# Performance work log

Measured on AMD Instinct MI355X. Metric: run time of the kernel, lower is better.

Reference implementation:

```python
import jax, jax.numpy as jnp
import numpy as np
from jax import lax

SCOPE = 15
RICKER_WIDTH = 3.0
DAMP = 0.12
MAX_STEPS = 10


def mexican_hat(scope, width, damping):
    # ricker / mexican-hat wavelet sampled at `scope` integer-spaced points, scaled by damping
    x = np.linspace(-(scope // 2), scope // 2, scope).astype(np.float32)
    norm = 2.0 / (np.sqrt(3.0 * width) * np.pi ** 0.25)
    w = damping * norm * (1.0 - (x / width) ** 2) * np.exp(-(x ** 2) / (2.0 * width ** 2))
    return jnp.asarray(w, dtype=jnp.float32)


def setup_inputs() -> dict:
    key = jax.random.key(0)
    activations = jax.random.normal(key, (32, 256, 56, 56), dtype=jnp.float32)
    w_rec = mexican_hat(SCOPE, RICKER_WIDTH, DAMP)  # [scope]
    return {"activations": activations, "w_rec": w_rec, "max_steps": MAX_STEPS}


def reference(activations, w_rec, max_steps):
    # activations: [B, C, H, W]; inhibition conv runs along the C axis only.
    scope = w_rec.shape[0]
    pad = scope // 2
    x = activations[:, None]                     # [B, 1, C, H, W]
    kernel = w_rec.reshape(1, 1, scope, 1, 1)    # OIDHW

    def conv(y):
        return lax.conv_general_dilated(
            y, kernel,
            window_strides=(1, 1, 1),
            padding=[(pad, pad), (0, 0), (0, 0)],
            dimension_numbers=("NCDHW", "OIDHW", "NCDHW"),
        )

    # fixed-point iteration: state <- activations + W_rec * state  (threshold=0 => always max_steps iters)
    state = x
    for _ in range(max_steps):
        state = x + conv(state)
    return state[:, 0]  # squeeze channel dim -> [B, C, H, W]
```

## Files before the change

kernel.cpp:

```cpp
#include <hip/hip_runtime.h>


#define NCH 256
#define PAD 7
#define SCOPE 15
#define SPATIAL 3136
#define PER_B 802816
#define STW 32
#define STILES_PER_B 98
#define NTILES 3136
#define GRID_APPLY 512
#define MAXCH 12

typedef __attribute__((ext_vector_type(8))) __bf16 bf16x8;
typedef __attribute__((ext_vector_type(16))) float float16;
typedef __attribute__((ext_vector_type(4))) unsigned int uint4v;

static __device__ __forceinline__ unsigned short f2bf_rn_u(float f) {
  unsigned u = __builtin_bit_cast(unsigned int, f);
  return (unsigned short)((u + 0x7FFFu + ((u >> 16) & 1u)) >> 16);
}
static __device__ __forceinline__ float bf2f_u(unsigned short h) {
  unsigned u = ((unsigned)h) << 16;
  return __builtin_bit_cast(float, u);
}
static __device__ __forceinline__ unsigned pack_bf2(float a, float b) {
  return (unsigned)f2bf_rn_u(a) | ((unsigned)f2bf_rn_u(b) << 16);
}
static __device__ __forceinline__ void split2(float a, float b,
                                              unsigned& h, unsigned& l) {
  h = pack_bf2(a, b);
  const float ra = a - __builtin_bit_cast(float, h << 16);
  const float rb = b - __builtin_bit_cast(float, h & 0xFFFF0000u);
  l = pack_bf2(ra, rb);
}

__global__ void build_M_kernel(const float* __restrict__ w,
                               const int* __restrict__ max_steps_p,
                               unsigned short* __restrict__ Mh,
                               unsigned short* __restrict__ Ml) {
  const int d = blockIdx.x;
  const int c = threadIdx.x;
  __shared__ float v[2][NCH];
  __shared__ float wsh[SCOPE];
  if (c < SCOPE) wsh[c] = w[c];
  const float e = (c == d) ? 1.0f : 0.0f;
  v[0][c] = e;
  __syncthreads();
  const int steps = *max_steps_p;
  int cur = 0;
  for (int t = 0; t < steps; ++t) {
    float s = e;
#pragma unroll
    for (int j = 0; j < SCOPE; ++j) {
      const int cc = c + j - PAD;
      if (cc >= 0 && cc < NCH) s += wsh[j] * v[cur][cc];
    }
    cur ^= 1;
    v[cur][c] = s;
    __syncthreads();
  }
  const float f = v[cur][c];
  const unsigned short h = f2bf_rn_u(f);
  Mh[c * NCH + d] = h;
  Ml[c * NCH + d] = f2bf_rn_u(f - bf2f_u(h));
}

__global__ __launch_bounds__(512, 4) void apply_M_kernel(
    const float* __restrict__ x, const unsigned short* __restrict__ Mh,
    const unsigned short* __restrict__ Ml, float* __restrict__ out) {
  __shared__ unsigned HB[128 * STW];
  __shared__ unsigned LB[128 * STW];

  const int tid  = threadIdx.x;
  const int lane = tid & 63;
  const int w    = tid >> 6;
  const int m    = lane & 31;
  const int half = lane >> 5;
  const int c0   = w * 32;

  int clo = c0 - 70; if (clo < 0) clo = 0; clo >>= 4;
  int chi = c0 + 101; if (chi > 255) chi = 255; chi >>= 4;
  const int nch = chi - clo + 1;

  const unsigned short* mh = Mh + (c0 + m) * NCH + clo * 16 + half * 8;
  const unsigned short* ml = Ml + (c0 + m) * NCH + clo * 16 + half * 8;

  const int sq = (tid & 7) * 4;
  const int dg = tid >> 3;

  int tau = blockIdx.x;
  float4 g0, g1, g2, g3;
  {
    const float* gb = x + (size_t)(tau / STILES_PER_B) * PER_B
                        + (size_t)(tau % STILES_PER_B) * STW;
    g0 = *(const float4*)(gb + (size_t)(2 * dg) * SPATIAL + sq);
    g1 = *(const float4*)(gb + (size_t)(2 * dg + 1) * SPATIAL + sq);
    g2 = *(const float4*)(gb + (size_t)(2 * dg + 128) * SPATIAL + sq);
    g3 = *(const float4*)(gb + (size_t)(2 * dg + 129) * SPATIAL + sq);
  }

#pragma unroll 1
  for (; tau < NTILES; tau += GRID_APPLY) {
    __syncthreads();

    {
      unsigned h0, h1, h2, h3, l0, l1, l2, l3;
      split2(g0.x, g1.x, h0, l0); split2(g0.y, g1.y, h1, l1);
      split2(g0.z, g1.z, h2, l2); split2(g0.w, g1.w, h3, l3);
      *(uint4v*)&HB[dg * STW + sq] = (uint4v){h0, h1, h2, h3};
      *(uint4v*)&LB[dg * STW + sq] = (uint4v){l0, l1, l2, l3};
      split2(g2.x, g3.x, h0, l0); split2(g2.y, g3.y, h1, l1);
      split2(g2.z, g3.z, h2, l2); split2(g2.w, g3.w, h3, l3);
      *(uint4v*)&HB[(dg + 64) * STW + sq] = (uint4v){h0, h1, h2, h3};
      *(uint4v*)&LB[(dg + 64) * STW + sq] = (uint4v){l0, l1, l2, l3};
    }

    const int ntau = tau + GRID_APPLY;
    if (ntau < NTILES) {
      const float* gb = x + (size_t)(ntau / STILES_PER_B) * PER_B
                          + (size_t)(ntau % STILES_PER_B) * STW;
      g0 = *(const float4*)(gb + (size_t)(2 * dg) * SPATIAL + sq);
      g1 = *(const float4*)(gb + (size_t)(2 * dg + 1) * SPATIAL + sq);
      g2 = *(const float4*)(gb + (size_t)(2 * dg + 128) * SPATIAL + sq);
      g3 = *(const float4*)(gb + (size_t)(2 * dg + 129) * SPATIAL + sq);
    }

    __syncthreads();

    const unsigned short* mhp = mh;
    const unsigned short* mlp = ml;
    asm volatile("" : "+v"(mhp), "+v"(mlp));

    float16 a0, a1;
#pragma unroll
    for (int q = 0; q < 16; ++q) { a0[q] = 0.0f; a1[q] = 0.0f; }

#pragma unroll
    for (int i = 0; i < MAXCH; ++i) {
      if (i < nch) {
        const bf16x8 Ah = *(const bf16x8*)(mhp + i * 16);
        const bf16x8 Al = *(const bf16x8*)(mlp + i * 16);
        const int k2b = (clo + i) * 8 + half * 4;
        const unsigned* hp = &HB[k2b * STW + m];
        const unsigned* lp = &LB[k2b * STW + m];
        const uint4v hw = {hp[0], hp[32], hp[64], hp[96]};
        const uint4v lw = {lp[0], lp[32], lp[64], lp[96]};
        const bf16x8 bh = __builtin_bit_cast(bf16x8, hw);
        const bf16x8 bl = __builtin_bit_cast(bf16x8, lw);
        a0 = __builtin_amdgcn_mfma_f32_32x32x16_bf16(Ah, bh, a0, 0, 0, 0);
        a1 = __builtin_amdgcn_mfma_f32_32x32x16_bf16(Ah, bl, a1, 0, 0, 0);
        a1 = __builtin_amdgcn_mfma_f32_32x32x16_bf16(Al, bh, a1, 0, 0, 0);
      }
    }

    const int b  = tau / STILES_PER_B;
    const int s0 = (tau % STILES_PER_B) * STW;
    float* ob = out + (size_t)b * PER_B + (size_t)s0 + m;
#pragma unroll
    for (int r = 0; r < 16; ++r) {
      const int row = (r & 3) + 8 * (r >> 2) + 4 * half;
      ob[(size_t)(c0 + row) * SPATIAL] = a0[r] + a1[r];
    }
  }
}

extern "C" void kernel_launch(void* const* d_in, const int* in_sizes, int n_in,
                              void* d_out, int out_size, void* d_ws, size_t ws_size,
                              hipStream_t stream) {
  const float* x = (const float*)d_in[0];
  const float* w = (const float*)d_in[1];
  const int* ms = (const int*)d_in[2];
  float* out = (float*)d_out;

  unsigned short* Mh = (unsigned short*)d_ws;
  unsigned short* Ml = Mh + NCH * NCH;

  build_M_kernel<<<NCH, NCH, 0, stream>>>(w, ms, Mh, Ml);
  apply_M_kernel<<<GRID_APPLY, 512, 0, stream>>>(x, Mh, Ml, out);
}
```

Before: 246.3 us.

## Double-buffer LDS tile, interleave hi/lo bf16 planes, prefetch M fragments

Replaces the separate high and low bf16 LDS planes with one interleaved buffer, so each B-operand row is read with 64-bit LDS loads instead of scalar ones. The buffer is double-buffered with a ping-pong offset, which removes the leading barrier of each tile iteration and leaves a single raw s_barrier after an lgkmcnt wait. The M operand fragments for the next k-chunk are loaded one iteration ahead to hide global/L2 latency behind the MFMAs. This doubles the LDS footprint to 64 KB per block, which may lower occupancy. It also drops vmcnt waiting at the barrier, relying on the compiler for the global-load ordering.

```diff
diff --git a/kernel.cpp b/kernel.cpp
--- a/kernel.cpp
+++ b/kernel.cpp
@@ -11,10 +11,12 @@
 #define NTILES 3136
 #define GRID_APPLY 512
 #define MAXCH 12
+#define BUFW 8192
 
 typedef __attribute__((ext_vector_type(8))) __bf16 bf16x8;
 typedef __attribute__((ext_vector_type(16))) float float16;
 typedef __attribute__((ext_vector_type(4))) unsigned int uint4v;
+typedef __attribute__((ext_vector_type(2))) unsigned int uint2v;
 
 static __device__ __forceinline__ unsigned short f2bf_rn_u(float f) {
   unsigned u = __builtin_bit_cast(unsigned int, f);
@@ -69,8 +71,7 @@
 __global__ __launch_bounds__(512, 4) void apply_M_kernel(
     const float* __restrict__ x, const unsigned short* __restrict__ Mh,
     const unsigned short* __restrict__ Ml, float* __restrict__ out) {
-  __shared__ unsigned HB[128 * STW];
-  __shared__ unsigned LB[128 * STW];
+  __shared__ unsigned XB[2 * BUFW];
 
   const int tid  = threadIdx.x;
   const int lane = tid & 63;
@@ -90,6 +91,7 @@
   const int dg = tid >> 3;
 
   int tau = blockIdx.x;
+  int bo = 0;
   float4 g0, g1, g2, g3;
   {
     const float* gb = x + (size_t)(tau / STILES_PER_B) * PER_B
@@ -102,18 +104,18 @@
 
 #pragma unroll 1
   for (; tau < NTILES; tau += GRID_APPLY) {
-    __syncthreads();
-
     {
       unsigned h0, h1, h2, h3, l0, l1, l2, l3;
       split2(g0.x, g1.x, h0, l0); split2(g0.y, g1.y, h1, l1);
       split2(g0.z, g1.z, h2, l2); split2(g0.w, g1.w, h3, l3);
-      *(uint4v*)&HB[dg * STW + sq] = (uint4v){h0, h1, h2, h3};
-      *(uint4v*)&LB[dg * STW + sq] = (uint4v){l0, l1, l2, l3};
+      unsigned* p = &XB[bo + dg * 64 + sq * 2];
+      *(uint4v*)(p)     = (uint4v){h0, l0, h1, l1};
+      *(uint4v*)(p + 4) = (uint4v){h2, l2, h3, l3};
       split2(g2.x, g3.x, h0, l0); split2(g2.y, g3.y, h1, l1);
       split2(g2.z, g3.z, h2, l2); split2(g2.w, g3.w, h3, l3);
-      *(uint4v*)&HB[(dg + 64) * STW + sq] = (uint4v){h0, h1, h2, h3};
-      *(uint4v*)&LB[(dg + 64) * STW + sq] = (uint4v){l0, l1, l2, l3};
+      unsigned* q = &XB[bo + (dg + 64) * 64 + sq * 2];
+      *(uint4v*)(q)     = (uint4v){h0, l0, h1, l1};
+      *(uint4v*)(q + 4) = (uint4v){h2, l2, h3, l3};
     }
 
     const int ntau = tau + GRID_APPLY;
@@ -126,7 +128,8 @@
       g3 = *(const float4*)(gb + (size_t)(2 * dg + 129) * SPATIAL + sq);
     }
 
-    __syncthreads();
+    asm volatile("s_waitcnt lgkmcnt(0)" ::: "memory");
+    __builtin_amdgcn_s_barrier();
 
     const unsigned short* mhp = mh;
     const unsigned short* mlp = ml;
@@ -136,21 +139,30 @@
 #pragma unroll
     for (int q = 0; q < 16; ++q) { a0[q] = 0.0f; a1[q] = 0.0f; }
 
+    bf16x8 cAh = *(const bf16x8*)(mhp);
+    bf16x8 cAl = *(const bf16x8*)(mlp);
 #pragma unroll
     for (int i = 0; i < MAXCH; ++i) {
       if (i < nch) {
-        const bf16x8 Ah = *(const bf16x8*)(mhp + i * 16);
-        const bf16x8 Al = *(const bf16x8*)(mlp + i * 16);
+        bf16x8 nAh, nAl;
+        if (i + 1 < nch) {
+          nAh = *(const bf16x8*)(mhp + (i + 1) * 16);
+          nAl = *(const bf16x8*)(mlp + (i + 1) * 16);
+        }
         const int k2b = (clo + i) * 8 + half * 4;
-        const unsigned* hp = &HB[k2b * STW + m];
-        const unsigned* lp = &LB[k2b * STW + m];
-        const uint4v hw = {hp[0], hp[32], hp[64], hp[96]};
-        const uint4v lw = {lp[0], lp[32], lp[64], lp[96]};
+        const unsigned* bp = &XB[bo + k2b * 64 + 2 * m];
+        const uint2v r0 = *(const uint2v*)(bp);
+        const uint2v r1 = *(const uint2v*)(bp + 64);
+        const uint2v r2 = *(const uint2v*)(bp + 128);
+        const uint2v r3 = *(const uint2v*)(bp + 192);
+        const uint4v hw = {r0.x, r1.x, r2.x, r3.x};
+        const uint4v lw = {r0.y, r1.y, r2.y, r3.y};
         const bf16x8 bh = __builtin_bit_cast(bf16x8, hw);
         const bf16x8 bl = __builtin_bit_cast(bf16x8, lw);
-        a0 = __builtin_amdgcn_mfma_f32_32x32x16_bf16(Ah, bh, a0, 0, 0, 0);
-        a1 = __builtin_amdgcn_mfma_f32_32x32x16_bf16(Ah, bl, a1, 0, 0, 0);
-        a1 = __builtin_amdgcn_mfma_f32_32x32x16_bf16(Al, bh, a1, 0, 0, 0);
+        a0 = __builtin_amdgcn_mfma_f32_32x32x16_bf16(cAh, bh, a0, 0, 0, 0);
+        a1 = __builtin_amdgcn_mfma_f32_32x32x16_bf16(cAh, bl, a1, 0, 0, 0);
+        a1 = __builtin_amdgcn_mfma_f32_32x32x16_bf16(cAl, bh, a1, 0, 0, 0);
+        cAh = nAh; cAl = nAl;
       }
     }
 
@@ -162,6 +174,8 @@
       const int row = (r & 3) + 8 * (r >> 2) + 4 * half;
       ob[(size_t)(c0 + row) * SPATIAL] = a0[r] + a1[r];
     }
+
+    bo ^= BUFW;
   }
 }
 
```

After: 249.2 us. About the same (+1.2%).
